# Kernel optimization log

Hardware: AMD Instinct MI355X
Metric: run time of the kernel (lower is better)

The kernel has to match this reference:

```python
import jax, jax.numpy as jnp
import numpy as np
import math

B_TOPK = 8  # self.B
NEG = -1e9  # numerically-equivalent stand-in for float('-inf') mask


def setup_inputs() -> dict:
    key = jax.random.key(0)
    ks = jax.random.split(key, 12)
    b, s, d, d_low = 4, 2048, 128, 16
    sc = 1.0 / math.sqrt(d)
    return {
        "queries": jax.random.normal(ks[0], (b, s, d), jnp.float32),
        "keys": jax.random.normal(ks[1], (b, s, d), jnp.float32),
        "values": jax.random.normal(ks[2], (b, s, d), jnp.float32),
        "valid_lens": jax.random.randint(ks[3], (b, s), 0, s, jnp.int32),
        "Wq_low": jax.random.normal(ks[4], (d, d_low), jnp.float32) * sc,
        "bq_low": jnp.zeros((d_low,), jnp.float32),
        "Wk_low": jax.random.normal(ks[5], (d, d_low), jnp.float32) * sc,
        "bk_low": jnp.zeros((d_low,), jnp.float32),
        "Wq_high": jax.random.normal(ks[6], (d, d_low), jnp.float32) * sc,
        "bq_high": jnp.zeros((d_low,), jnp.float32),
        "Wk_high": jax.random.normal(ks[7], (d, d_low), jnp.float32) * sc,
        "bk_high": jnp.zeros((d_low,), jnp.float32),
    }


def reference(queries, keys, values, valid_lens, Wq_low, bq_low, Wk_low, bk_low,
              Wq_high, bq_high, Wk_high, bk_high):
    b, s, d = queries.shape
    d_low = Wq_low.shape[1]
    scale = 1.0 / math.sqrt(d_low)

    # low-rank scores [b, sq, sk]
    q_low = queries @ Wq_low + bq_low
    k_low = keys @ Wk_low + bk_low
    scores_low = jnp.einsum('bqe,bke->bqk', q_low, k_low) * scale

    # mask: scatter -inf at (batch, valid_lens[b,k], k) along dim 1 (as in torch code)
    vl = jnp.clip(valid_lens, 0, s - 1)                      # [b, sk]
    mask = vl[:, None, :] == jnp.arange(s)[None, :, None]    # [b, sq, sk]
    scores_masked = jnp.where(mask, scores_low + NEG, scores_low)

    # top-B keys per query row (over key axis)
    _, topk_idx = jax.lax.top_k(scores_masked, B_TOPK)       # [b, s, B]

    # gather top-B queries/keys per row, project to d_low, rank-d_low correction score
    bi = jnp.arange(b)[:, None, None]
    q_high = queries[bi, topk_idx]                           # [b, s, B, d]
    k_high = keys[bi, topk_idx]                              # [b, s, B, d]
    q_proj = q_high @ Wq_high + bq_high                      # [b, s, B, d_low]
    k_proj = k_high @ Wk_high + bk_high
    score_high = jnp.sum(q_proj * k_proj, axis=-1) * scale   # [b, s, B]

    # scatter corrected scores back into the masked score matrix (dim 2)
    si = jnp.arange(s)[None, :, None]
    corrected = scores_masked.at[bi, si, topk_idx].set(score_high)

    # masked_softmax with valid_lens applies softmax over dim=1
    attn = jax.nn.softmax(corrected, axis=1)
    return jnp.einsum('bqk,bkd->bqd', attn, values)
```

## Files before the change

kernel.cpp:

```cpp
#include <hip/hip_runtime.h>
#include <float.h>
#include <math.h>

#define SEQ 2048
#define NB 4
#define DIM 128
#define DL 16
#define NEGV (-1e9f)
#define TOPK 8

#define QT 128
#define KC 64
#define QCH 64

typedef unsigned long long u64;
typedef __attribute__((ext_vector_type(8))) short short8;
typedef __attribute__((ext_vector_type(4))) float f32x4;

__device__ __forceinline__ void top8_insert(float* s, float key) {
    #pragma unroll
    for (int i = 0; i < 8; ++i) {
        float a = s[i];
        s[i] = fmaxf(a, key);
        key  = fminf(a, key);
    }
}

__device__ __forceinline__ float top8_merge16(float* s) {
    #pragma unroll
    for (int off = 1; off < 16; off <<= 1) {
        float o[8], t[8];
        #pragma unroll
        for (int i = 0; i < 8; ++i)
            o[i] = __shfl_xor(s[i], off, 64);
        #pragma unroll
        for (int i = 0; i < 8; ++i)
            t[i] = fmaxf(s[i], o[7 - i]);
        #pragma unroll
        for (int i = 0; i < 4; ++i) {
            float a = t[i], c = t[i + 4];
            t[i] = fmaxf(a, c); t[i + 4] = fminf(a, c);
        }
        #pragma unroll
        for (int g2 = 0; g2 < 8; g2 += 4) {
            float a = t[g2], c = t[g2 + 2];
            t[g2] = fmaxf(a, c); t[g2 + 2] = fminf(a, c);
            a = t[g2 + 1]; c = t[g2 + 3];
            t[g2 + 1] = fmaxf(a, c); t[g2 + 3] = fminf(a, c);
        }
        #pragma unroll
        for (int g1 = 0; g1 < 8; g1 += 2) {
            float a = t[g1], c = t[g1 + 1];
            t[g1] = fmaxf(a, c); t[g1 + 1] = fminf(a, c);
        }
        #pragma unroll
        for (int i = 0; i < 8; ++i) s[i] = t[i];
    }
    return s[7];
}

__device__ __forceinline__ unsigned bf16_rne(float x) {
    unsigned u = __float_as_uint(x);
    return (u + 0x7FFFu + ((u >> 16) & 1u)) >> 16;
}

__global__ __launch_bounds__(256) void proj_kernel(
    const float* __restrict__ q, const float* __restrict__ k,
    const float* __restrict__ Wql, const float* __restrict__ bql,
    const float* __restrict__ Wkl, const float* __restrict__ bkl,
    const float* __restrict__ Wqh, const float* __restrict__ bqh,
    const float* __restrict__ Wkh, const float* __restrict__ bkh,
    unsigned short* __restrict__ qA1, unsigned short* __restrict__ qA2,
    unsigned short* __restrict__ qA3,
    unsigned short* __restrict__ kB1, unsigned short* __restrict__ kB2,
    float* __restrict__ sh)
{
    __shared__ float Ws[4][DIM * DL];
    __shared__ float rowq[16][DIM];
    __shared__ float rowk[16][DIM];
    int tid = threadIdx.x;
    for (int i = tid; i < DIM * DL; i += 256) {
        Ws[0][i] = Wql[i];
        Ws[1][i] = Wkl[i];
        Ws[2][i] = Wqh[i];
        Ws[3][i] = Wkh[i];
    }
    int r0 = blockIdx.x * 16;
    for (int i = tid; i < 16 * DIM; i += 256) {
        int rr = i >> 7, cc = i & 127;
        rowq[rr][cc] = q[(size_t)(r0 + rr) * DIM + cc];
        rowk[rr][cc] = k[(size_t)(r0 + rr) * DIM + cc];
    }
    __syncthreads();
    int g = tid >> 4;
    int e = tid & 15;
    float aql = 0.f, akl = 0.f, aqh = 0.f, akh = 0.f;
    #pragma unroll 8
    for (int i = 0; i < DIM; ++i) {
        float qv = rowq[g][i], kv = rowk[g][i];
        aql = fmaf(qv, Ws[0][i * DL + e], aql);
        akl = fmaf(kv, Ws[1][i * DL + e], akl);
        aqh = fmaf(qv, Ws[2][i * DL + e], aqh);
        akh = fmaf(kv, Ws[3][i * DL + e], akh);
    }
    int t = r0 + g;
    float qv = aql + bql[e];
    float kv = akl + bkl[e];

    unsigned q1 = bf16_rne(qv);
    float q1f = __uint_as_float(q1 << 16);
    float qr1 = qv - q1f;
    unsigned q2 = bf16_rne(qr1);
    float q2f = __uint_as_float(q2 << 16);
    unsigned q3 = bf16_rne(qr1 - q2f);

    unsigned k1 = bf16_rne(kv);
    float k1f = __uint_as_float(k1 << 16);
    float kr1 = kv - k1f;
    unsigned k2 = bf16_rne(kr1);
    float k2f = __uint_as_float(k2 << 16);
    unsigned k3 = bf16_rne(kr1 - k2f);

    size_t pb = (size_t)t * 32;
    qA1[pb + e] = (unsigned short)q1; qA1[pb + 16 + e] = (unsigned short)q2;
    qA2[pb + e] = (unsigned short)q2; qA2[pb + 16 + e] = (unsigned short)q1;
    qA3[pb + e] = (unsigned short)q1; qA3[pb + 16 + e] = (unsigned short)q3;
    kB1[pb + e] = (unsigned short)k1; kB1[pb + 16 + e] = (unsigned short)k2;
    kB2[pb + e] = (unsigned short)k3; kB2[pb + 16 + e] = (unsigned short)k1;

    float qp = aqh + bqh[e];
    float kp = akh + bkh[e];
    float prod = qp * kp;
    #pragma unroll
    for (int off = 8; off >= 1; off >>= 1)
        prod += __shfl_xor(prod, off, 16);
    if (e == 0) sh[t] = 0.25f * prod;
}

__global__ __launch_bounds__(256) void vsplit_kernel(
    const float* __restrict__ V, unsigned short* __restrict__ VH,
    unsigned short* __restrict__ VL)
{
    __shared__ float T[32][33];
    int kb = blockIdx.x * 32, db = blockIdx.y * 32, b = blockIdx.z;
    int tid = threadIdx.x;
    {
        int r = tid >> 3, cg = tid & 7;
        float4 v = *(const float4*)(V + ((size_t)b * SEQ + kb + r) * DIM + db + cg * 4);
        T[r][cg * 4 + 0] = v.x; T[r][cg * 4 + 1] = v.y;
        T[r][cg * 4 + 2] = v.z; T[r][cg * 4 + 3] = v.w;
    }
    __syncthreads();
    int dr = tid >> 3, kg = tid & 7;
    unsigned h[4], l[4];
    #pragma unroll
    for (int j = 0; j < 4; ++j) {
        float f = T[kg * 4 + j][dr];
        unsigned hi = bf16_rne(f);
        float hf = __uint_as_float(hi << 16);
        unsigned lo = bf16_rne(f - hf);
        h[j] = hi; l[j] = lo;
    }
    size_t o = ((size_t)b * DIM + db + dr) * SEQ + kb + kg * 4;
    *(uint2*)(VH + o) = make_uint2(h[0] | (h[1] << 16), h[2] | (h[3] << 16));
    *(uint2*)(VL + o) = make_uint2(l[0] | (l[1] << 16), l[2] | (l[3] << 16));
}

__global__ __launch_bounds__(256) void score_mfma(
    const unsigned short* __restrict__ qA1, const unsigned short* __restrict__ qA2,
    const unsigned short* __restrict__ qA3,
    const unsigned short* __restrict__ kB1, const unsigned short* __restrict__ kB2,
    const int* __restrict__ valid_lens, const float* __restrict__ sh,
    float* __restrict__ Smat, float* __restrict__ thrv,
    float2* __restrict__ pml, int do_stats)
{
    __shared__ float red[4][16][8];
    __shared__ float thr_s[16];

    int tid  = threadIdx.x;
    int lane = tid & 63;
    int wv   = tid >> 6;
    int c15  = lane & 15;
    int g    = lane >> 4;
    int row0 = __builtin_amdgcn_readfirstlane(blockIdx.x * 16);
    int b    = row0 >> 11;
    int qi0  = row0 & (SEQ - 1);

    size_t aoff = (size_t)(row0 + c15) * 32 + g * 8;
    short8 A1 = *(const short8*)(qA1 + aoff);
    short8 A2 = *(const short8*)(qA2 + aoff);
    short8 A3 = *(const short8*)(qA3 + aoff);

    const unsigned short* kb1 = kB1 + (size_t)b * SEQ * 32;
    const unsigned short* kb2 = kB2 + (size_t)b * SEQ * 32;
    const int* vlb = valid_lens + (size_t)b * SEQ;

    float s8[4][8];
    #pragma unroll
    for (int r = 0; r < 4; ++r)
        #pragma unroll
        for (int i = 0; i < 8; ++i) s8[r][i] = -FLT_MAX;

    int rowg[4];
    #pragma unroll
    for (int r = 0; r < 4; ++r) rowg[r] = qi0 + g * 4 + r;

    float s_reg[32][4];

    #pragma unroll
    for (int t = 0; t < 32; ++t) {
        int ct  = wv * 32 + t;
        int col = ct * 16 + c15;
        size_t boff = (size_t)col * 32 + g * 8;
        short8 B1 = *(const short8*)(kb1 + boff);
        short8 B2 = *(const short8*)(kb2 + boff);

        f32x4 acc = (f32x4){0.f, 0.f, 0.f, 0.f};
        acc = __builtin_amdgcn_mfma_f32_16x16x32_bf16(A1, B1, acc, 0, 0, 0);
        acc = __builtin_amdgcn_mfma_f32_16x16x32_bf16(A2, B1, acc, 0, 0, 0);
        acc = __builtin_amdgcn_mfma_f32_16x16x32_bf16(A3, B2, acc, 0, 0, 0);

        int vl = vlb[col];
        vl = vl < 0 ? 0 : (vl > SEQ - 1 ? SEQ - 1 : vl);

        float* So = Smat + (size_t)(row0 + g * 4) * SEQ + col;
        #pragma unroll
        for (int r = 0; r < 4; ++r) {
            float v = 0.25f * acc[r];
            if (vl == rowg[r]) v += NEGV;
            So[(size_t)r * SEQ] = v;
            s_reg[t][r] = v;
            top8_insert(s8[r], v);
        }
    }

    #pragma unroll
    for (int r = 0; r < 4; ++r) top8_merge16(s8[r]);

    if (c15 == 0) {
        #pragma unroll
        for (int r = 0; r < 4; ++r)
            #pragma unroll
            for (int i = 0; i < 8; ++i)
                red[wv][g * 4 + r][i] = s8[r][i];
    }
    __syncthreads();
    if (tid < 16) {
        float fin[8];
        #pragma unroll
        for (int i = 0; i < 8; ++i) fin[i] = red[0][tid][i];
        #pragma unroll
        for (int w2 = 1; w2 < 4; ++w2)
            #pragma unroll
            for (int i = 0; i < 8; ++i)
                top8_insert(fin, red[w2][tid][i]);
        thrv[row0 + tid] = fin[7];
        thr_s[tid] = fin[7];
    }

    if (!do_stats) return;
    __syncthreads();

    const float* shb = sh + (size_t)b * SEQ;
    int chunk = qi0 >> 4;
    float thr_l[4];
    #pragma unroll
    for (int r = 0; r < 4; ++r) thr_l[r] = thr_s[g * 4 + r];

    #pragma unroll
    for (int t = 0; t < 32; ++t) {
        int col = (wv * 32 + t) * 16 + c15;
        float shk = shb[col];
        float m = -FLT_MAX, l = 0.f;
        #pragma unroll
        for (int r = 0; r < 4; ++r) {
            float v = s_reg[t][r];
            v = (v >= thr_l[r]) ? shk : v;
            float nm = fmaxf(m, v);
            l = l * __expf(m - nm) + __expf(v - nm);
            m = nm;
        }
        #pragma unroll
        for (int off = 16; off <= 32; off <<= 1) {
            float mo = __shfl_xor(m, off, 64);
            float lo = __shfl_xor(l, off, 64);
            float nm = fmaxf(m, mo);
            l = l * __expf(m - nm) + lo * __expf(mo - nm);
            m = nm;
        }
        if (g == 0)
            pml[((size_t)b * 128 + chunk) * SEQ + col] = make_float2(m, l);
    }
}

__global__ __launch_bounds__(256) void colred_final2(
    const float2* __restrict__ pml,
    float* __restrict__ cmax, float* __restrict__ cinv)
{
    __shared__ float2 red[4][64];
    int tid = threadIdx.x;
    int c0 = tid & 63, sl = tid >> 6;
    int gcol = blockIdx.x * 64 + c0;
    int b = gcol >> 11, kcol = gcol & (SEQ - 1);
    float m = -FLT_MAX, l = 0.f;
    #pragma unroll 8
    for (int i = 0; i < 32; ++i) {
        int c = sl * 32 + i;
        float2 p = pml[((size_t)b * 128 + c) * SEQ + kcol];
        float nm = fmaxf(m, p.x);
        l = l * __expf(m - nm) + p.y * __expf(p.x - nm);
        m = nm;
    }
    red[sl][c0] = make_float2(m, l);
    __syncthreads();
    if (sl == 0) {
        #pragma unroll
        for (int s = 1; s < 4; ++s) {
            float2 p = red[s][c0];
            float nm = fmaxf(m, p.x);
            l = l * __expf(m - nm) + p.y * __expf(p.x - nm);
            m = nm;
        }
        cmax[gcol] = m;
        cinv[gcol] = 1.f / l;
    }
}

__global__ __launch_bounds__(256) void colred_partial(
    const float* __restrict__ Smat, const float* __restrict__ thrv,
    const float* __restrict__ sh,
    float* __restrict__ pm, float* __restrict__ pl)
{
    int kcol = blockIdx.x * 256 + threadIdx.x;
    int qc = blockIdx.y;
    int b  = blockIdx.z;
    const float* Sp  = Smat + (size_t)b * SEQ * SEQ + (size_t)(qc * QCH) * SEQ + kcol;
    const float* thb = thrv + (size_t)b * SEQ + qc * QCH;
    float shk = sh[(size_t)b * SEQ + kcol];
    float m = -FLT_MAX, l = 0.f;
    #pragma unroll 4
    for (int qq = 0; qq < QCH; ++qq) {
        float v = Sp[(size_t)qq * SEQ];
        float t = thb[qq];
        v = (v >= t) ? shk : v;
        float nm = fmaxf(m, v);
        l = l * __expf(m - nm) + __expf(v - nm);
        m = nm;
    }
    pm[((size_t)b * 32 + qc) * SEQ + kcol] = m;
    pl[((size_t)b * 32 + qc) * SEQ + kcol] = l;
}

__global__ __launch_bounds__(256) void colred_final(
    const float* __restrict__ pm, const float* __restrict__ pl,
    float* __restrict__ cmax, float* __restrict__ cinv)
{
    int idx = blockIdx.x * 256 + threadIdx.x;
    int b = idx >> 11, kcol = idx & (SEQ - 1);
    float m = -FLT_MAX, l = 0.f;
    #pragma unroll
    for (int c = 0; c < 32; ++c) {
        float mm = pm[((size_t)b * 32 + c) * SEQ + kcol];
        float ll = pl[((size_t)b * 32 + c) * SEQ + kcol];
        float nm = fmaxf(m, mm);
        l = l * __expf(m - nm) + ll * __expf(mm - nm);
        m = nm;
    }
    cmax[idx] = m;
    cinv[idx] = 1.f / l;
}

__global__ __launch_bounds__(256) void out_mfma(
    const float* __restrict__ Smat, const unsigned short* __restrict__ VH,
    const unsigned short* __restrict__ VL,
    const float* __restrict__ cmax, const float* __restrict__ cinv,
    const float* __restrict__ thrv, const float* __restrict__ sh,
    float* __restrict__ dst, int krange)
{
    __shared__ unsigned int VtH[DIM * 32];
    __shared__ unsigned int VtL[DIM * 32];

    int tid  = threadIdx.x;
    int w    = tid >> 6;
    int lane = tid & 63;
    int ln   = lane & 15;
    int quad = lane >> 4;
    int q0   = blockIdx.x * QT;
    int ksid = blockIdx.y;
    int b    = blockIdx.z;
    int kbeg = ksid * krange;

    const float* Sb = Smat + (size_t)b * SEQ * SEQ;
    const unsigned short* VHb = VH + (size_t)b * DIM * SEQ;
    const unsigned short* VLb = VL + (size_t)b * DIM * SEQ;
    const float* cm  = cmax + (size_t)b * SEQ;
    const float* ci  = cinv + (size_t)b * SEQ;
    const float* shb = sh + (size_t)b * SEQ;

    float thrm[2];
    #pragma unroll
    for (int mt = 0; mt < 2; ++mt)
        thrm[mt] = thrv[(size_t)b * SEQ + q0 + w * 32 + mt * 16 + ln];

    f32x4 acc[2][8];
    #pragma unroll
    for (int mt = 0; mt < 2; ++mt)
        #pragma unroll
        for (int nt = 0; nt < 8; ++nt)
            acc[mt][nt] = (f32x4){0.f, 0.f, 0.f, 0.f};

    int sd0   = tid >> 3;
    int skseg = tid & 7;

    for (int k0 = kbeg; k0 < kbeg + krange; k0 += KC) {
        #pragma unroll
        for (int it = 0; it < 4; ++it) {
            int d = sd0 + it * 32;
            size_t go = (size_t)d * SEQ + k0 + skseg * 8;
            uint4 hv = *(const uint4*)(VHb + go);
            uint4 lv = *(const uint4*)(VLb + go);
            int wa = d * 32 + ((skseg ^ (d & 7)) << 2);
            *(uint4*)&VtH[wa] = hv;
            *(uint4*)&VtL[wa] = lv;
        }

        short8 Ah[2][2], Al[2][2];
        #pragma unroll
        for (int ks = 0; ks < 2; ++ks) {
            int kk = k0 + ks * 32 + quad * 8;
            float4 cma = *(const float4*)(cm + kk);
            float4 cmb = *(const float4*)(cm + kk + 4);
            float4 cia = *(const float4*)(ci + kk);
            float4 cib = *(const float4*)(ci + kk + 4);
            float4 sha = *(const float4*)(shb + kk);
            float4 shx = *(const float4*)(shb + kk + 4);
            #pragma unroll
            for (int mt = 0; mt < 2; ++mt) {
                const float* Sp = Sb + (size_t)(q0 + w * 32 + mt * 16 + ln) * SEQ + kk;
                float4 sa = *(const float4*)Sp;
                float4 sb = *(const float4*)(Sp + 4);
                float t = thrm[mt];
                float e0 = (sa.x >= t) ? sha.x : sa.x;
                float e1 = (sa.y >= t) ? sha.y : sa.y;
                float e2 = (sa.z >= t) ? sha.z : sa.z;
                float e3 = (sa.w >= t) ? sha.w : sa.w;
                float e4 = (sb.x >= t) ? shx.x : sb.x;
                float e5 = (sb.y >= t) ? shx.y : sb.y;
                float e6 = (sb.z >= t) ? shx.z : sb.z;
                float e7 = (sb.w >= t) ? shx.w : sb.w;
                float p[8];
                p[0] = __expf(e0 - cma.x) * cia.x;
                p[1] = __expf(e1 - cma.y) * cia.y;
                p[2] = __expf(e2 - cma.z) * cia.z;
                p[3] = __expf(e3 - cma.w) * cia.w;
                p[4] = __expf(e4 - cmb.x) * cib.x;
                p[5] = __expf(e5 - cmb.y) * cib.y;
                p[6] = __expf(e6 - cmb.z) * cib.z;
                p[7] = __expf(e7 - cmb.w) * cib.w;
                #pragma unroll
                for (int j = 0; j < 8; ++j) {
                    unsigned hi = bf16_rne(p[j]);
                    float hf = __uint_as_float(hi << 16);
                    unsigned lo = bf16_rne(p[j] - hf);
                    Ah[mt][ks][j] = (short)hi;
                    Al[mt][ks][j] = (short)lo;
                }
            }
        }
        __syncthreads();

        #pragma unroll
        for (int nt = 0; nt < 8; ++nt) {
            int d = nt * 16 + ln;
            #pragma unroll
            for (int ks = 0; ks < 2; ++ks) {
                int kseg = ks * 4 + quad;
                int wa = d * 32 + ((kseg ^ (d & 7)) << 2);
                short8 bh = *(short8*)&VtH[wa];
                short8 bl = *(short8*)&VtL[wa];
                #pragma unroll
                for (int mt = 0; mt < 2; ++mt) {
                    acc[mt][nt] = __builtin_amdgcn_mfma_f32_16x16x32_bf16(
                        Ah[mt][ks], bh, acc[mt][nt], 0, 0, 0);
                    acc[mt][nt] = __builtin_amdgcn_mfma_f32_16x16x32_bf16(
                        Al[mt][ks], bh, acc[mt][nt], 0, 0, 0);
                    acc[mt][nt] = __builtin_amdgcn_mfma_f32_16x16x32_bf16(
                        Ah[mt][ks], bl, acc[mt][nt], 0, 0, 0);
                }
            }
        }
        __syncthreads();
    }

    float* dp = dst + (size_t)ksid * ((size_t)NB * SEQ * DIM)
                    + (size_t)b * SEQ * DIM;
    #pragma unroll
    for (int mt = 0; mt < 2; ++mt) {
        #pragma unroll
        for (int r = 0; r < 4; ++r) {
            float* o = dp + (size_t)(q0 + w * 32 + mt * 16 + quad * 4 + r) * DIM + ln;
            #pragma unroll
            for (int nt = 0; nt < 8; ++nt)
                o[nt * 16] = acc[mt][nt][r];
        }
    }
}

__global__ __launch_bounds__(256) void reduce_kernel(
    const float* __restrict__ part, float* __restrict__ out, int ksplit)
{
    int idx = blockIdx.x * 256 + threadIdx.x;
    const float4* p = (const float4*)part;
    float4 a = p[idx];
    for (int s = 1; s < ksplit; ++s) {
        float4 q = p[(size_t)idx + (size_t)s * 262144];
        a.x += q.x; a.y += q.y; a.z += q.z; a.w += q.w;
    }
    ((float4*)out)[idx] = a;
}

extern "C" void kernel_launch(void* const* d_in, const int* in_sizes, int n_in,
                              void* d_out, int out_size, void* d_ws, size_t ws_size,
                              hipStream_t stream)
{
    const float* queries = (const float*)d_in[0];
    const float* keys    = (const float*)d_in[1];
    const float* values  = (const float*)d_in[2];
    const int*   valid   = (const int*)d_in[3];
    const float* Wql = (const float*)d_in[4];
    const float* bql = (const float*)d_in[5];
    const float* Wkl = (const float*)d_in[6];
    const float* bkl = (const float*)d_in[7];
    const float* Wqh = (const float*)d_in[8];
    const float* bqh = (const float*)d_in[9];
    const float* Wkh = (const float*)d_in[10];
    const float* bkh = (const float*)d_in[11];

    char* ws = (char*)d_ws;
    float* Smat = (float*)(ws);
    unsigned short* qA1 = (unsigned short*)(ws + 67108864);
    unsigned short* qA2 = (unsigned short*)(ws + 67633152);
    unsigned short* qA3 = (unsigned short*)(ws + 68157440);
    unsigned short* kB1 = (unsigned short*)(ws + 68681728);
    unsigned short* kB2 = (unsigned short*)(ws + 69206016);
    float* sh    = (float*)(ws + 69730304);
    float* thrv  = (float*)(ws + 69763072);
    float* cmax  = (float*)(ws + 69795840);
    float* cinv  = (float*)(ws + 69828608);
    unsigned short* VthH = (unsigned short*)(ws + 69861376);
    unsigned short* VthL = (unsigned short*)(ws + 71958528);
    const size_t part_off = 74055680;
    float2* pml  = (float2*)(ws + part_off);
    float* pm    = (float*)(ws + part_off);
    float* pl    = (float*)(ws + part_off + 1048576);
    float* part  = (float*)(ws + part_off);

    const size_t part_sz  = (size_t)NB * SEQ * DIM * 4;
    int ksplit = 1;
    if      (ws_size >= part_off + 8 * part_sz) ksplit = 8;
    else if (ws_size >= part_off + 4 * part_sz) ksplit = 4;
    else if (ws_size >= part_off + 2 * part_sz) ksplit = 2;

    int fused = (ws_size >= part_off + 8388608) ? 1 : 0;

    proj_kernel<<<dim3((NB * SEQ) / 16), 256, 0, stream>>>(
        queries, keys, Wql, bql, Wkl, bkl, Wqh, bqh, Wkh, bkh,
        qA1, qA2, qA3, kB1, kB2, sh);

    vsplit_kernel<<<dim3(SEQ / 32, DIM / 32, NB), 256, 0, stream>>>(
        values, VthH, VthL);

    score_mfma<<<dim3((NB * SEQ) / 16), 256, 0, stream>>>(
        qA1, qA2, qA3, kB1, kB2, valid, sh, Smat, thrv, pml, fused);

    if (fused) {
        colred_final2<<<dim3((NB * SEQ) / 64), 256, 0, stream>>>(pml, cmax, cinv);
    } else {
        colred_partial<<<dim3(SEQ / 256, 32, NB), 256, 0, stream>>>(
            Smat, thrv, sh, pm, pl);
        colred_final<<<dim3((NB * SEQ) / 256), 256, 0, stream>>>(pm, pl, cmax, cinv);
    }

    if (ksplit == 1) {
        out_mfma<<<dim3(SEQ / QT, 1, NB), 256, 0, stream>>>(
            Smat, VthH, VthL, cmax, cinv, thrv, sh, (float*)d_out, SEQ);
    } else {
        out_mfma<<<dim3(SEQ / QT, ksplit, NB), 256, 0, stream>>>(
            Smat, VthH, VthL, cmax, cinv, thrv, sh, part, SEQ / ksplit);
        reduce_kernel<<<(NB * SEQ * DIM / 4) / 256, 256, 0, stream>>>(
            part, (float*)d_out, ksplit);
    }
}
```

Baseline: 186.4 us.

## Recompute scores in second pass and store corrected scores, dropping threshold arrays

The score kernel no longer keeps a 32x4 per-thread register array of scores across the top-k reduction. After the threshold is known it recomputes the MFMA scores and writes the already-corrected values (top-8 entries replaced by the high-rank score) into the score matrix. The column-reduction and output kernels then read corrected scores directly and skip the threshold and sh loads and selects. This cuts register pressure and per-element work downstream, at the cost of running the score MFMAs and K loads twice.

Result: faster. 168.5 us (-9.6%).

```diff
diff --git a/kernel.cpp b/kernel.cpp
--- a/kernel.cpp
+++ b/kernel.cpp
@@ -171,8 +171,7 @@
     const unsigned short* __restrict__ qA3,
     const unsigned short* __restrict__ kB1, const unsigned short* __restrict__ kB2,
     const int* __restrict__ valid_lens, const float* __restrict__ sh,
-    float* __restrict__ Smat, float* __restrict__ thrv,
-    float2* __restrict__ pml, int do_stats)
+    float* __restrict__ Smat, float2* __restrict__ pml, int do_stats)
 {
     __shared__ float red[4][16][8];
     __shared__ float thr_s[16];
@@ -205,12 +204,9 @@
     #pragma unroll
     for (int r = 0; r < 4; ++r) rowg[r] = qi0 + g * 4 + r;
 
-    float s_reg[32][4];
-
     #pragma unroll
     for (int t = 0; t < 32; ++t) {
-        int ct  = wv * 32 + t;
-        int col = ct * 16 + c15;
+        int col = (wv * 32 + t) * 16 + c15;
         size_t boff = (size_t)col * 32 + g * 8;
         short8 B1 = *(const short8*)(kb1 + boff);
         short8 B2 = *(const short8*)(kb2 + boff);
@@ -223,13 +219,10 @@
         int vl = vlb[col];
         vl = vl < 0 ? 0 : (vl > SEQ - 1 ? SEQ - 1 : vl);
 
-        float* So = Smat + (size_t)(row0 + g * 4) * SEQ + col;
         #pragma unroll
         for (int r = 0; r < 4; ++r) {
             float v = 0.25f * acc[r];
             if (vl == rowg[r]) v += NEGV;
-            So[(size_t)r * SEQ] = v;
-            s_reg[t][r] = v;
             top8_insert(s8[r], v);
         }
     }
@@ -254,11 +247,8 @@
             #pragma unroll
             for (int i = 0; i < 8; ++i)
                 top8_insert(fin, red[w2][tid][i]);
-        thrv[row0 + tid] = fin[7];
         thr_s[tid] = fin[7];
     }
-
-    if (!do_stats) return;
     __syncthreads();
 
     const float* shb = sh + (size_t)b * SEQ;
@@ -270,26 +260,43 @@
     #pragma unroll
     for (int t = 0; t < 32; ++t) {
         int col = (wv * 32 + t) * 16 + c15;
+        size_t boff = (size_t)col * 32 + g * 8;
+        short8 B1 = *(const short8*)(kb1 + boff);
+        short8 B2 = *(const short8*)(kb2 + boff);
+
+        f32x4 acc = (f32x4){0.f, 0.f, 0.f, 0.f};
+        acc = __builtin_amdgcn_mfma_f32_16x16x32_bf16(A1, B1, acc, 0, 0, 0);
+        acc = __builtin_amdgcn_mfma_f32_16x16x32_bf16(A2, B1, acc, 0, 0, 0);
+        acc = __builtin_amdgcn_mfma_f32_16x16x32_bf16(A3, B2, acc, 0, 0, 0);
+
+        int vl = vlb[col];
+        vl = vl < 0 ? 0 : (vl > SEQ - 1 ? SEQ - 1 : vl);
         float shk = shb[col];
+
+        float* So = Smat + (size_t)(row0 + g * 4) * SEQ + col;
         float m = -FLT_MAX, l = 0.f;
         #pragma unroll
         for (int r = 0; r < 4; ++r) {
-            float v = s_reg[t][r];
+            float v = 0.25f * acc[r];
+            if (vl == rowg[r]) v += NEGV;
             v = (v >= thr_l[r]) ? shk : v;
+            So[(size_t)r * SEQ] = v;
             float nm = fmaxf(m, v);
             l = l * __expf(m - nm) + __expf(v - nm);
             m = nm;
         }
-        #pragma unroll
-        for (int off = 16; off <= 32; off <<= 1) {
-            float mo = __shfl_xor(m, off, 64);
-            float lo = __shfl_xor(l, off, 64);
-            float nm = fmaxf(m, mo);
-            l = l * __expf(m - nm) + lo * __expf(mo - nm);
-            m = nm;
-        }
-        if (g == 0)
-            pml[((size_t)b * 128 + chunk) * SEQ + col] = make_float2(m, l);
+        if (do_stats) {
+            #pragma unroll
+            for (int off = 16; off <= 32; off <<= 1) {
+                float mo = __shfl_xor(m, off, 64);
+                float lo = __shfl_xor(l, off, 64);
+                float nm = fmaxf(m, mo);
+                l = l * __expf(m - nm) + lo * __expf(mo - nm);
+                m = nm;
+            }
+            if (g == 0)
+                pml[((size_t)b * 128 + chunk) * SEQ + col] = make_float2(m, l);
+        }
     }
 }
 
@@ -327,22 +334,16 @@
 }
 
 __global__ __launch_bounds__(256) void colred_partial(
-    const float* __restrict__ Smat, const float* __restrict__ thrv,
-    const float* __restrict__ sh,
-    float* __restrict__ pm, float* __restrict__ pl)
+    const float* __restrict__ Smat, float* __restrict__ pm, float* __restrict__ pl)
 {
     int kcol = blockIdx.x * 256 + threadIdx.x;
     int qc = blockIdx.y;
     int b  = blockIdx.z;
-    const float* Sp  = Smat + (size_t)b * SEQ * SEQ + (size_t)(qc * QCH) * SEQ + kcol;
-    const float* thb = thrv + (size_t)b * SEQ + qc * QCH;
-    float shk = sh[(size_t)b * SEQ + kcol];
+    const float* Sp = Smat + (size_t)b * SEQ * SEQ + (size_t)(qc * QCH) * SEQ + kcol;
     float m = -FLT_MAX, l = 0.f;
     #pragma unroll 4
     for (int qq = 0; qq < QCH; ++qq) {
         float v = Sp[(size_t)qq * SEQ];
-        float t = thb[qq];
-        v = (v >= t) ? shk : v;
         float nm = fmaxf(m, v);
         l = l * __expf(m - nm) + __expf(v - nm);
         m = nm;
@@ -374,7 +375,6 @@
     const float* __restrict__ Smat, const unsigned short* __restrict__ VH,
     const unsigned short* __restrict__ VL,
     const float* __restrict__ cmax, const float* __restrict__ cinv,
-    const float* __restrict__ thrv, const float* __restrict__ sh,
     float* __restrict__ dst, int krange)
 {
     __shared__ unsigned int VtH[DIM * 32];
@@ -395,12 +395,6 @@
     const unsigned short* VLb = VL + (size_t)b * DIM * SEQ;
     const float* cm  = cmax + (size_t)b * SEQ;
     const float* ci  = cinv + (size_t)b * SEQ;
-    const float* shb = sh + (size_t)b * SEQ;
-
-    float thrm[2];
-    #pragma unroll
-    for (int mt = 0; mt < 2; ++mt)
-        thrm[mt] = thrv[(size_t)b * SEQ + q0 + w * 32 + mt * 16 + ln];
 
     f32x4 acc[2][8];
     #pragma unroll
@@ -432,31 +426,20 @@
             float4 cmb = *(const float4*)(cm + kk + 4);
             float4 cia = *(const float4*)(ci + kk);
             float4 cib = *(const float4*)(ci + kk + 4);
-            float4 sha = *(const float4*)(shb + kk);
-            float4 shx = *(const float4*)(shb + kk + 4);
             #pragma unroll
             for (int mt = 0; mt < 2; ++mt) {
                 const float* Sp = Sb + (size_t)(q0 + w * 32 + mt * 16 + ln) * SEQ + kk;
                 float4 sa = *(const float4*)Sp;
                 float4 sb = *(const float4*)(Sp + 4);
-                float t = thrm[mt];
-                float e0 = (sa.x >= t) ? sha.x : sa.x;
-                float e1 = (sa.y >= t) ? sha.y : sa.y;
-                float e2 = (sa.z >= t) ? sha.z : sa.z;
-                float e3 = (sa.w >= t) ? sha.w : sa.w;
-                float e4 = (sb.x >= t) ? shx.x : sb.x;
-                float e5 = (sb.y >= t) ? shx.y : sb.y;
-                float e6 = (sb.z >= t) ? shx.z : sb.z;
-                float e7 = (sb.w >= t) ? shx.w : sb.w;
                 float p[8];
-                p[0] = __expf(e0 - cma.x) * cia.x;
-                p[1] = __expf(e1 - cma.y) * cia.y;
-                p[2] = __expf(e2 - cma.z) * cia.z;
-                p[3] = __expf(e3 - cma.w) * cia.w;
-                p[4] = __expf(e4 - cmb.x) * cib.x;
-                p[5] = __expf(e5 - cmb.y) * cib.y;
-                p[6] = __expf(e6 - cmb.z) * cib.z;
-                p[7] = __expf(e7 - cmb.w) * cib.w;
+                p[0] = __expf(sa.x - cma.x) * cia.x;
+                p[1] = __expf(sa.y - cma.y) * cia.y;
+                p[2] = __expf(sa.z - cma.z) * cia.z;
+                p[3] = __expf(sa.w - cma.w) * cia.w;
+                p[4] = __expf(sb.x - cmb.x) * cib.x;
+                p[5] = __expf(sb.y - cmb.y) * cib.y;
+                p[6] = __expf(sb.z - cmb.z) * cib.z;
+                p[7] = __expf(sb.w - cmb.w) * cib.w;
                 #pragma unroll
                 for (int j = 0; j < 8; ++j) {
                     unsigned hi = bf16_rne(p[j]);
@@ -544,7 +527,6 @@
     unsigned short* kB1 = (unsigned short*)(ws + 68681728);
     unsigned short* kB2 = (unsigned short*)(ws + 69206016);
     float* sh    = (float*)(ws + 69730304);
-    float* thrv  = (float*)(ws + 69763072);
     float* cmax  = (float*)(ws + 69795840);
     float* cinv  = (float*)(ws + 69828608);
     unsigned short* VthH = (unsigned short*)(ws + 69861376);
@@ -571,22 +553,21 @@
         values, VthH, VthL);
 
     score_mfma<<<dim3((NB * SEQ) / 16), 256, 0, stream>>>(
-        qA1, qA2, qA3, kB1, kB2, valid, sh, Smat, thrv, pml, fused);
+        qA1, qA2, qA3, kB1, kB2, valid, sh, Smat, pml, fused);
 
     if (fused) {
         colred_final2<<<dim3((NB * SEQ) / 64), 256, 0, stream>>>(pml, cmax, cinv);
     } else {
-        colred_partial<<<dim3(SEQ / 256, 32, NB), 256, 0, stream>>>(
-            Smat, thrv, sh, pm, pl);
+        colred_partial<<<dim3(SEQ / 256, 32, NB), 256, 0, stream>>>(Smat, pm, pl);
         colred_final<<<dim3((NB * SEQ) / 256), 256, 0, stream>>>(pm, pl, cmax, cinv);
     }
 
     if (ksplit == 1) {
         out_mfma<<<dim3(SEQ / QT, 1, NB), 256, 0, stream>>>(
-            Smat, VthH, VthL, cmax, cinv, thrv, sh, (float*)d_out, SEQ);
+            Smat, VthH, VthL, cmax, cinv, (float*)d_out, SEQ);
     } else {
         out_mfma<<<dim3(SEQ / QT, ksplit, NB), 256, 0, stream>>>(
-            Smat, VthH, VthL, cmax, cinv, thrv, sh, part, SEQ / ksplit);
+            Smat, VthH, VthL, cmax, cinv, part, SEQ / ksplit);
         reduce_kernel<<<(NB * SEQ * DIM / 4) / 256, 256, 0, stream>>>(
             part, (float*)d_out, ksplit);
     }
```
